# Kernel optimization log

Hardware: AMD Instinct MI355X
Metric: run time of the kernel (lower is better)

The kernel has to match this reference:

```python
import jax, jax.numpy as jnp
import numpy as np

EMBED_DIM = 1024
NUM_HEADS = 16
HEAD_DIM = EMBED_DIM // NUM_HEADS


def setup_inputs() -> dict:
    key = jax.random.key(0)
    k1, k2, k3, k4, k5 = jax.random.split(key, 5)
    x = jax.random.normal(k1, (4, 2048, EMBED_DIM), dtype=jnp.float32)
    # nn.Linear params: weight [out, in], bias [out]
    s_in = 1.0 / np.sqrt(EMBED_DIM)
    W_qkv = jax.random.uniform(k2, (3 * EMBED_DIM, EMBED_DIM), jnp.float32, -s_in, s_in)
    b_qkv = jax.random.uniform(k3, (3 * EMBED_DIM,), jnp.float32, -s_in, s_in)
    W_out = jax.random.uniform(k4, (EMBED_DIM, EMBED_DIM), jnp.float32, -s_in, s_in)
    b_out = jax.random.uniform(k5, (EMBED_DIM,), jnp.float32, -s_in, s_in)
    return {"x": x, "W_qkv": W_qkv, "b_qkv": b_qkv, "W_out": W_out, "b_out": b_out}


def reference(x, W_qkv, b_qkv, W_out, b_out):
    B, S, D = x.shape
    H, Dh = NUM_HEADS, HEAD_DIM
    qkv = x @ W_qkv.T + b_qkv                      # [B, S, 3D]
    qkv = qkv.reshape(B, S, 3, H, Dh)
    q = qkv[:, :, 0].transpose(0, 2, 1, 3)        # [B, H, S, Dh]
    k = qkv[:, :, 1].transpose(0, 2, 1, 3)
    v = qkv[:, :, 2].transpose(0, 2, 1, 3)
    scale = 1.0 / jnp.sqrt(jnp.asarray(Dh, x.dtype))
    scores = jnp.einsum('bhqd,bhkd->bhqk', q, k) * scale  # [B, H, S, S]
    attn = jax.nn.softmax(scores, axis=-1)
    out = jnp.einsum('bhqk,bhkd->bhqd', attn, v)  # [B, H, S, Dh]
    out = out.transpose(0, 2, 1, 3).reshape(B, S, D)
    return out @ W_out.T + b_out
```

## Files before the change

kernel.cpp:

```cpp
#include <hip/hip_runtime.h>

#define BB 4
#define SS 2048
#define DD 1024
#define HH 16
#define DHH 64
#define MM (BB*SS)

typedef __bf16 bf16x8 __attribute__((ext_vector_type(8)));
typedef float  f32x4  __attribute__((ext_vector_type(4)));

__device__ __forceinline__ unsigned short f2bf(float x) {
    unsigned int u = __float_as_uint(x);
    u += 0x7FFFu + ((u >> 16) & 1u);
    return (unsigned short)(u >> 16);
}

__global__ __launch_bounds__(256) void cvt_all(
    const float4* __restrict__ x,  const float4* __restrict__ wq,
    const float4* __restrict__ wo,
    ushort4* __restrict__ xb, ushort4* __restrict__ wqb, ushort4* __restrict__ wob)
{
    int i = blockIdx.x * 256 + threadIdx.x;
    const float4* src; ushort4* dst; int j;
    if (i < 2097152)      { src = x;  dst = xb;  j = i; }
    else if (i < 2883584) { src = wq; dst = wqb; j = i - 2097152; }
    else                  { src = wo; dst = wob; j = i - 2883584; }
    float4 v = src[j];
    ushort4 o;
    o.x = f2bf(v.x); o.y = f2bf(v.y); o.z = f2bf(v.z); o.w = f2bf(v.w);
    dst[j] = o;
}

__global__ __launch_bounds__(256) void qkv_gemm(
    const __bf16* __restrict__ A,
    const __bf16* __restrict__ W,
    const float* __restrict__ bias,
    __bf16* __restrict__ Qp,
    __bf16* __restrict__ Kp,
    __bf16* __restrict__ Vp)
{
    __shared__ __bf16 smem[2 * 128 * 72];
#define AS(r,c) smem[(r)*72 + (c)]
#define BS(r,c) smem[128*72 + (r)*72 + (c)]
#define CT(r,c) smem[(r)*132 + (c)]
    const int tid  = threadIdx.x;
    const int m0   = blockIdx.x * 128;
    const int n0   = blockIdx.y * 128;
    const int lane = tid & 63;
    const int wid  = tid >> 6;
    const int fr   = lane & 15;
    const int quad = lane >> 4;
    const int wm   = (wid >> 1) * 64;
    const int wn   = (wid & 1) * 64;

    f32x4 acc[4][4] = {};

    for (int k0 = 0; k0 < DD; k0 += 64) {
        __syncthreads();
        #pragma unroll
        for (int p = 0; p < 4; ++p) {
            int g = tid + p * 256;
            int r = g >> 3;
            int c = (g & 7) << 3;
            *(uint4*)&AS(r, c) = *(const uint4*)(A + (size_t)(m0 + r) * DD + k0 + c);
            *(uint4*)&BS(r, c) = *(const uint4*)(W + (size_t)(n0 + r) * DD + k0 + c);
        }
        __syncthreads();

        bf16x8 af[2][4], bw[2][4];
        #pragma unroll
        for (int kc = 0; kc < 2; ++kc)
            #pragma unroll
            for (int t = 0; t < 4; ++t) {
                af[kc][t] = *(const bf16x8*)&AS(wm + t*16 + fr, kc*32 + quad*8);
                bw[kc][t] = *(const bf16x8*)&BS(wn + t*16 + fr, kc*32 + quad*8);
            }
        #pragma unroll
        for (int kc = 0; kc < 2; ++kc)
            #pragma unroll
            for (int mt = 0; mt < 4; ++mt)
                #pragma unroll
                for (int nt = 0; nt < 4; ++nt)
                    acc[mt][nt] = __builtin_amdgcn_mfma_f32_16x16x32_bf16(
                        af[kc][mt], bw[kc][nt], acc[mt][nt], 0, 0, 0);
    }

    __syncthreads();
    const int t3 = n0 >> 10;
    const int b  = m0 >> 11;
    const int s0 = m0 & (SS - 1);

    float bn[4];
    #pragma unroll
    for (int nt = 0; nt < 4; ++nt) bn[nt] = bias[n0 + wn + nt*16 + fr];

    if (t3 == 2) {
        #pragma unroll
        for (int nt = 0; nt < 4; ++nt)
            #pragma unroll
            for (int mt = 0; mt < 4; ++mt)
                #pragma unroll
                for (int i = 0; i < 4; ++i)
                    CT(wn + nt*16 + fr, wm + mt*16 + quad*4 + i) =
                        (__bf16)(acc[mt][nt][i] + bn[nt]);
        __syncthreads();
        const int pn0 = n0 - 2048;
        #pragma unroll
        for (int p = 0; p < 8; ++p) {
            int g = tid + p * 256;
            int r = g >> 4;
            int c = (g & 15) << 3;
            int pn = pn0 + r, h = pn >> 6, dh = pn & 63;
            *(uint4*)&Vp[((size_t)((b*HH + h)*DHH + dh))*SS + s0 + c] = *(uint4*)&CT(r, c);
        }
    } else {
        __bf16* dst = (t3 == 0) ? Qp : Kp;
        const float qscale = (t3 == 0) ? 0.125f : 1.0f;
        #pragma unroll
        for (int nt = 0; nt < 4; ++nt)
            #pragma unroll
            for (int mt = 0; mt < 4; ++mt)
                #pragma unroll
                for (int i = 0; i < 4; ++i)
                    CT(wm + mt*16 + quad*4 + i, wn + nt*16 + fr) =
                        (__bf16)((acc[mt][nt][i] + bn[nt]) * qscale);
        __syncthreads();
        const int pn0 = (t3 == 0) ? n0 : n0 - 1024;
        #pragma unroll
        for (int p = 0; p < 8; ++p) {
            int g = tid + p * 256;
            int r = g >> 4;
            int c = (g & 15) << 3;
            int pn = pn0 + c, h = pn >> 6, dh = pn & 63;
            *(uint4*)&dst[((size_t)((b*HH + h))*SS + s0 + r)*DHH + dh] = *(uint4*)&CT(r, c);
        }
    }
#undef AS
#undef BS
#undef CT
}

__global__ __launch_bounds__(256) void out_gemm(
    const __bf16* __restrict__ A,
    const __bf16* __restrict__ W,
    const float* __restrict__ bias,
    float* __restrict__ out)
{
    __shared__ __bf16 As[128][72];
    __shared__ __bf16 Bs[128][72];
    const int tid  = threadIdx.x;
    const int m0   = blockIdx.x * 128;
    const int n0   = blockIdx.y * 128;
    const int lane = tid & 63;
    const int wid  = tid >> 6;
    const int fr   = lane & 15;
    const int quad = lane >> 4;
    const int wm   = (wid >> 1) * 64;
    const int wn   = (wid & 1) * 64;

    f32x4 acc[4][4] = {};

    for (int k0 = 0; k0 < DD; k0 += 64) {
        __syncthreads();
        #pragma unroll
        for (int p = 0; p < 4; ++p) {
            int g = tid + p * 256;
            int r = g >> 3;
            int c = (g & 7) << 3;
            *(uint4*)&As[r][c] = *(const uint4*)(A + (size_t)(m0 + r) * DD + k0 + c);
            *(uint4*)&Bs[r][c] = *(const uint4*)(W + (size_t)(n0 + r) * DD + k0 + c);
        }
        __syncthreads();

        bf16x8 af[2][4], bw[2][4];
        #pragma unroll
        for (int kc = 0; kc < 2; ++kc)
            #pragma unroll
            for (int t = 0; t < 4; ++t) {
                af[kc][t] = *(const bf16x8*)&As[wm + t*16 + fr][kc*32 + quad*8];
                bw[kc][t] = *(const bf16x8*)&Bs[wn + t*16 + fr][kc*32 + quad*8];
            }
        #pragma unroll
        for (int kc = 0; kc < 2; ++kc)
            #pragma unroll
            for (int mt = 0; mt < 4; ++mt)
                #pragma unroll
                for (int nt = 0; nt < 4; ++nt)
                    acc[mt][nt] = __builtin_amdgcn_mfma_f32_16x16x32_bf16(
                        af[kc][mt], bw[kc][nt], acc[mt][nt], 0, 0, 0);
    }

    #pragma unroll
    for (int nt = 0; nt < 4; ++nt) {
        int n  = n0 + wn + nt*16 + fr;
        float bnv = bias[n];
        #pragma unroll
        for (int mt = 0; mt < 4; ++mt) {
            #pragma unroll
            for (int i = 0; i < 4; ++i) {
                int m = m0 + wm + mt*16 + quad*4 + i;
                out[(size_t)m * DD + n] = acc[mt][nt][i] + bnv;
            }
        }
    }
}

__global__ __launch_bounds__(256, 2) void attn_mfma(
    const __bf16* __restrict__ Qp,
    const __bf16* __restrict__ Kp,
    const __bf16* __restrict__ Vp,
    __bf16* __restrict__ Op)
{
    __shared__ __bf16 Ks[128][72];
    __shared__ __bf16 VT[64][136];
    __shared__ __bf16 QPs[256][72];

    const int tid  = threadIdx.x;
    const int q0   = blockIdx.x * 256;
    const int bh   = blockIdx.y;
    const size_t base = (size_t)bh * SS * DHH;
    const int lane = tid & 63;
    const int wid  = tid >> 6;
    const int fr   = lane & 15;
    const int quad = lane >> 4;
    const int wrow = wid * 64;

    #pragma unroll
    for (int p = 0; p < 8; ++p) {
        int g = tid + p * 256;
        int r = g >> 3;
        int c = (g & 7) << 3;
        *(uint4*)&QPs[r][c] = *(const uint4*)(Qp + base + (size_t)(q0 + r) * DHH + c);
    }
    __syncthreads();

    bf16x8 aq[4][2];
    #pragma unroll
    for (int mt = 0; mt < 4; ++mt)
        #pragma unroll
        for (int kc = 0; kc < 2; ++kc)
            aq[mt][kc] = *(const bf16x8*)&QPs[wrow + mt*16 + fr][kc*32 + quad*8];

    f32x4 o[4][4] = {};
    float lp[4][4] = {};

    for (int kt = 0; kt < SS; kt += 128) {
        __syncthreads();
        #pragma unroll
        for (int p = 0; p < 4; ++p) {
            int g  = tid + p * 256;
            int rk = g >> 3;
            int ck = (g & 7) << 3;
            *(uint4*)&Ks[rk][ck] = *(const uint4*)(Kp + base + (size_t)(kt + rk) * DHH + ck);
            int dv = g >> 4;
            int cv = (g & 15) << 3;
            *(uint4*)&VT[dv][cv] = *(const uint4*)(Vp + base + (size_t)dv * SS + kt + cv);
        }
        __syncthreads();

        #pragma unroll
        for (int half = 0; half < 2; ++half) {
            const int koff = half * 64;

            #pragma unroll
            for (int mt = 0; mt < 4; ++mt) {
                f32x4 s[4] = {};
                #pragma unroll
                for (int nt = 0; nt < 4; ++nt)
                    #pragma unroll
                    for (int kc = 0; kc < 2; ++kc) {
                        bf16x8 bk = *(const bf16x8*)&Ks[koff + nt*16 + fr][kc*32 + quad*8];
                        s[nt] = __builtin_amdgcn_mfma_f32_16x16x32_bf16(
                            aq[mt][kc], bk, s[nt], 0, 0, 0);
                    }
                #pragma unroll
                for (int i = 0; i < 4; ++i) {
                    float e0 = __expf(s[0][i]);
                    float e1 = __expf(s[1][i]);
                    float e2 = __expf(s[2][i]);
                    float e3 = __expf(s[3][i]);
                    lp[mt][i] += (e0 + e1) + (e2 + e3);
                    QPs[wrow + mt*16 + quad*4 + i][0*16 + fr] = (__bf16)e0;
                    QPs[wrow + mt*16 + quad*4 + i][1*16 + fr] = (__bf16)e1;
                    QPs[wrow + mt*16 + quad*4 + i][2*16 + fr] = (__bf16)e2;
                    QPs[wrow + mt*16 + quad*4 + i][3*16 + fr] = (__bf16)e3;
                }
            }

            #pragma unroll
            for (int mt = 0; mt < 4; ++mt) {
                bf16x8 ap[2];
                #pragma unroll
                for (int kc = 0; kc < 2; ++kc)
                    ap[kc] = *(const bf16x8*)&QPs[wrow + mt*16 + fr][kc*32 + quad*8];
                #pragma unroll
                for (int nt = 0; nt < 4; ++nt)
                    #pragma unroll
                    for (int kc = 0; kc < 2; ++kc) {
                        bf16x8 bv = *(const bf16x8*)&VT[nt*16 + fr][koff + kc*32 + quad*8];
                        o[mt][nt] = __builtin_amdgcn_mfma_f32_16x16x32_bf16(
                            ap[kc], bv, o[mt][nt], 0, 0, 0);
                    }
            }
        }
    }

    __syncthreads();
    #pragma unroll
    for (int mt = 0; mt < 4; ++mt)
        #pragma unroll
        for (int i = 0; i < 4; ++i) {
            float v = lp[mt][i];
            v += __shfl_xor(v, 1);
            v += __shfl_xor(v, 2);
            v += __shfl_xor(v, 4);
            v += __shfl_xor(v, 8);
            float inv = 1.0f / v;
            #pragma unroll
            for (int nt = 0; nt < 4; ++nt)
                QPs[wrow + mt*16 + quad*4 + i][nt*16 + fr] = (__bf16)(o[mt][nt][i] * inv);
        }
    __syncthreads();

    const int b = bh >> 4, h = bh & (HH - 1);
    #pragma unroll
    for (int p = 0; p < 8; ++p) {
        int g = tid + p * 256;
        int r = g >> 3;
        int c = (g & 7) << 3;
        *(uint4*)&Op[((size_t)(b*SS + q0 + r))*DD + h*DHH + c] = *(uint4*)&QPs[r][c];
    }
}


extern "C" void kernel_launch(void* const* d_in, const int* in_sizes, int n_in,
                              void* d_out, int out_size, void* d_ws, size_t ws_size,
                              hipStream_t stream)
{
    const float* x     = (const float*)d_in[0];
    const float* W_qkv = (const float*)d_in[1];
    const float* b_qkv = (const float*)d_in[2];
    const float* W_out = (const float*)d_in[3];
    const float* b_out = (const float*)d_in[4];
    float* out = (float*)d_out;

    __bf16* ws  = (__bf16*)d_ws;
    __bf16* xb  = ws;
    __bf16* wqb = xb  + (size_t)8388608;
    __bf16* wob = wqb + (size_t)3145728;
    __bf16* qp  = wob + (size_t)1048576;
    __bf16* kp  = qp  + (size_t)8388608;
    __bf16* vp  = kp  + (size_t)8388608;
    __bf16* op  = vp  + (size_t)8388608;

    cvt_all<<<12288, 256, 0, stream>>>(
        (const float4*)x, (const float4*)W_qkv, (const float4*)W_out,
        (ushort4*)xb, (ushort4*)wqb, (ushort4*)wob);

    qkv_gemm<<<dim3(MM/128, 3*DD/128), 256, 0, stream>>>(xb, wqb, b_qkv, qp, kp, vp);
    attn_mfma<<<dim3(SS/256, BB*HH), 256, 0, stream>>>(qp, kp, vp, op);
    out_gemm<<<dim3(MM/128, DD/128), 256, 0, stream>>>(op, wob, b_out, out);
}
```

Baseline: 316.1 us.

## Use direct global-to-LDS loads with XOR-swizzled tiles and exp2 softmax

Replaces register-staged global-to-shared copies in both GEMMs and the attention kernel with global_load_lds 16-byte direct transfers. The shared tiles move from padded rows to an unpadded, rotation-swizzled layout, and fragment reads use the matching swizzle to avoid bank conflicts. K and V fragments are hoisted out of the mt loop in attention. The log2(e) factor is folded into the Q scale so the softmax can use the hardware exp2. This cuts VGPR traffic and LDS reads, but it depends on the per-lane LDS address pattern of global_load_lds matching the swizzle.

```diff
diff --git a/kernel.cpp b/kernel.cpp
--- a/kernel.cpp
+++ b/kernel.cpp
@@ -14,6 +14,12 @@
     unsigned int u = __float_as_uint(x);
     u += 0x7FFFu + ((u >> 16) & 1u);
     return (unsigned short)(u >> 16);
+}
+
+__device__ __forceinline__ void glds16(const __bf16* g, __bf16* l) {
+    __builtin_amdgcn_global_load_lds(
+        (const __attribute__((address_space(1))) void*)g,
+        (__attribute__((address_space(3))) void*)l, 16, 0, 0);
 }
 
 __global__ __launch_bounds__(256) void cvt_all(
@@ -40,10 +46,10 @@
     __bf16* __restrict__ Kp,
     __bf16* __restrict__ Vp)
 {
-    __shared__ __bf16 smem[2 * 128 * 72];
-#define AS(r,c) smem[(r)*72 + (c)]
-#define BS(r,c) smem[128*72 + (r)*72 + (c)]
+    __shared__ __bf16 smem[16896];
 #define CT(r,c) smem[(r)*132 + (c)]
+    __bf16* As = smem;
+    __bf16* Bs = smem + 8192;
     const int tid  = threadIdx.x;
     const int m0   = blockIdx.x * 128;
     const int n0   = blockIdx.y * 128;
@@ -54,17 +60,19 @@
     const int wm   = (wid >> 1) * 64;
     const int wn   = (wid & 1) * 64;
 
+    const int srow = lane >> 3;
+    const int sg   = ((lane & 7) - srow) & 7;
+
     f32x4 acc[4][4] = {};
 
     for (int k0 = 0; k0 < DD; k0 += 64) {
         __syncthreads();
         #pragma unroll
         for (int p = 0; p < 4; ++p) {
-            int g = tid + p * 256;
-            int r = g >> 3;
-            int c = (g & 7) << 3;
-            *(uint4*)&AS(r, c) = *(const uint4*)(A + (size_t)(m0 + r) * DD + k0 + c);
-            *(uint4*)&BS(r, c) = *(const uint4*)(W + (size_t)(n0 + r) * DD + k0 + c);
+            int cidx = p * 4 + wid;
+            int r = cidx * 8 + srow;
+            glds16(A + (size_t)(m0 + r) * DD + k0 + sg * 8, As + cidx * 512);
+            glds16(W + (size_t)(n0 + r) * DD + k0 + sg * 8, Bs + cidx * 512);
         }
         __syncthreads();
 
@@ -73,8 +81,9 @@
         for (int kc = 0; kc < 2; ++kc)
             #pragma unroll
             for (int t = 0; t < 4; ++t) {
-                af[kc][t] = *(const bf16x8*)&AS(wm + t*16 + fr, kc*32 + quad*8);
-                bw[kc][t] = *(const bf16x8*)&BS(wn + t*16 + fr, kc*32 + quad*8);
+                int col = ((kc * 4 + quad + fr) & 7) * 8;
+                af[kc][t] = *(const bf16x8*)&As[(wm + t*16 + fr) * 64 + col];
+                bw[kc][t] = *(const bf16x8*)&Bs[(wn + t*16 + fr) * 64 + col];
             }
         #pragma unroll
         for (int kc = 0; kc < 2; ++kc)
@@ -116,7 +125,7 @@
         }
     } else {
         __bf16* dst = (t3 == 0) ? Qp : Kp;
-        const float qscale = (t3 == 0) ? 0.125f : 1.0f;
+        const float qscale = (t3 == 0) ? 0.125f * 1.44269504088896340736f : 1.0f;
         #pragma unroll
         for (int nt = 0; nt < 4; ++nt)
             #pragma unroll
@@ -136,8 +145,6 @@
             *(uint4*)&dst[((size_t)((b*HH + h))*SS + s0 + r)*DHH + dh] = *(uint4*)&CT(r, c);
         }
     }
-#undef AS
-#undef BS
 #undef CT
 }
 
@@ -147,8 +154,9 @@
     const float* __restrict__ bias,
     float* __restrict__ out)
 {
-    __shared__ __bf16 As[128][72];
-    __shared__ __bf16 Bs[128][72];
+    __shared__ __bf16 smem[16384];
+    __bf16* As = smem;
+    __bf16* Bs = smem + 8192;
     const int tid  = threadIdx.x;
     const int m0   = blockIdx.x * 128;
     const int n0   = blockIdx.y * 128;
@@ -159,17 +167,19 @@
     const int wm   = (wid >> 1) * 64;
     const int wn   = (wid & 1) * 64;
 
+    const int srow = lane >> 3;
+    const int sg   = ((lane & 7) - srow) & 7;
+
     f32x4 acc[4][4] = {};
 
     for (int k0 = 0; k0 < DD; k0 += 64) {
         __syncthreads();
         #pragma unroll
         for (int p = 0; p < 4; ++p) {
-            int g = tid + p * 256;
-            int r = g >> 3;
-            int c = (g & 7) << 3;
-            *(uint4*)&As[r][c] = *(const uint4*)(A + (size_t)(m0 + r) * DD + k0 + c);
-            *(uint4*)&Bs[r][c] = *(const uint4*)(W + (size_t)(n0 + r) * DD + k0 + c);
+            int cidx = p * 4 + wid;
+            int r = cidx * 8 + srow;
+            glds16(A + (size_t)(m0 + r) * DD + k0 + sg * 8, As + cidx * 512);
+            glds16(W + (size_t)(n0 + r) * DD + k0 + sg * 8, Bs + cidx * 512);
         }
         __syncthreads();
 
@@ -178,8 +188,9 @@
         for (int kc = 0; kc < 2; ++kc)
             #pragma unroll
             for (int t = 0; t < 4; ++t) {
-                af[kc][t] = *(const bf16x8*)&As[wm + t*16 + fr][kc*32 + quad*8];
-                bw[kc][t] = *(const bf16x8*)&Bs[wn + t*16 + fr][kc*32 + quad*8];
+                int col = ((kc * 4 + quad + fr) & 7) * 8;
+                af[kc][t] = *(const bf16x8*)&As[(wm + t*16 + fr) * 64 + col];
+                bw[kc][t] = *(const bf16x8*)&Bs[(wn + t*16 + fr) * 64 + col];
             }
         #pragma unroll
         for (int kc = 0; kc < 2; ++kc)
@@ -212,8 +223,8 @@
     const __bf16* __restrict__ Vp,
     __bf16* __restrict__ Op)
 {
-    __shared__ __bf16 Ks[128][72];
-    __shared__ __bf16 VT[64][136];
+    __shared__ __bf16 Ks[128 * 64];
+    __shared__ __bf16 VT[64 * 128];
     __shared__ __bf16 QPs[256][72];
 
     const int tid  = threadIdx.x;
@@ -226,6 +237,11 @@
     const int quad = lane >> 4;
     const int wrow = wid * 64;
 
+    const int srowK = lane >> 3;
+    const int sgK   = ((lane & 7) - srowK) & 7;
+    const int srowV = lane >> 4;
+    const int sgV0  = lane & 15;
+
     #pragma unroll
     for (int p = 0; p < 8; ++p) {
         int g = tid + p * 256;
@@ -249,13 +265,12 @@
         __syncthreads();
         #pragma unroll
         for (int p = 0; p < 4; ++p) {
-            int g  = tid + p * 256;
-            int rk = g >> 3;
-            int ck = (g & 7) << 3;
-            *(uint4*)&Ks[rk][ck] = *(const uint4*)(Kp + base + (size_t)(kt + rk) * DHH + ck);
-            int dv = g >> 4;
-            int cv = (g & 15) << 3;
-            *(uint4*)&VT[dv][cv] = *(const uint4*)(Vp + base + (size_t)dv * SS + kt + cv);
+            int cidx = p * 4 + wid;
+            int rk = cidx * 8 + srowK;
+            glds16(Kp + base + (size_t)(kt + rk) * DHH + sgK * 8, Ks + cidx * 512);
+            int rv = cidx * 4 + srowV;
+            int gv = (sgV0 - rv) & 15;
+            glds16(Vp + base + (size_t)rv * SS + kt + gv * 8, VT + cidx * 512);
         }
         __syncthreads();
 
@@ -263,23 +278,29 @@
         for (int half = 0; half < 2; ++half) {
             const int koff = half * 64;
 
+            bf16x8 bk[4][2];
+            #pragma unroll
+            for (int nt = 0; nt < 4; ++nt)
+                #pragma unroll
+                for (int kc = 0; kc < 2; ++kc)
+                    bk[nt][kc] = *(const bf16x8*)
+                        &Ks[(koff + nt*16 + fr) * 64 + ((kc*4 + quad + fr) & 7) * 8];
+
             #pragma unroll
             for (int mt = 0; mt < 4; ++mt) {
                 f32x4 s[4] = {};
                 #pragma unroll
                 for (int nt = 0; nt < 4; ++nt)
                     #pragma unroll
-                    for (int kc = 0; kc < 2; ++kc) {
-                        bf16x8 bk = *(const bf16x8*)&Ks[koff + nt*16 + fr][kc*32 + quad*8];
+                    for (int kc = 0; kc < 2; ++kc)
                         s[nt] = __builtin_amdgcn_mfma_f32_16x16x32_bf16(
-                            aq[mt][kc], bk, s[nt], 0, 0, 0);
-                    }
+                            aq[mt][kc], bk[nt][kc], s[nt], 0, 0, 0);
                 #pragma unroll
                 for (int i = 0; i < 4; ++i) {
-                    float e0 = __expf(s[0][i]);
-                    float e1 = __expf(s[1][i]);
-                    float e2 = __expf(s[2][i]);
-                    float e3 = __expf(s[3][i]);
+                    float e0 = __builtin_amdgcn_exp2f(s[0][i]);
+                    float e1 = __builtin_amdgcn_exp2f(s[1][i]);
+                    float e2 = __builtin_amdgcn_exp2f(s[2][i]);
+                    float e3 = __builtin_amdgcn_exp2f(s[3][i]);
                     lp[mt][i] += (e0 + e1) + (e2 + e3);
                     QPs[wrow + mt*16 + quad*4 + i][0*16 + fr] = (__bf16)e0;
                     QPs[wrow + mt*16 + quad*4 + i][1*16 + fr] = (__bf16)e1;
@@ -288,6 +309,14 @@
                 }
             }
 
+            bf16x8 bv[4][2];
+            #pragma unroll
+            for (int nt = 0; nt < 4; ++nt)
+                #pragma unroll
+                for (int kc = 0; kc < 2; ++kc)
+                    bv[nt][kc] = *(const bf16x8*)
+                        &VT[(nt*16 + fr) * 128 + ((half*8 + kc*4 + quad + fr) & 15) * 8];
+
             #pragma unroll
             for (int mt = 0; mt < 4; ++mt) {
                 bf16x8 ap[2];
@@ -297,11 +326,9 @@
                 #pragma unroll
                 for (int nt = 0; nt < 4; ++nt)
                     #pragma unroll
-                    for (int kc = 0; kc < 2; ++kc) {
-                        bf16x8 bv = *(const bf16x8*)&VT[nt*16 + fr][koff + kc*32 + quad*8];
+                    for (int kc = 0; kc < 2; ++kc)
                         o[mt][nt] = __builtin_amdgcn_mfma_f32_16x16x32_bf16(
-                            ap[kc], bv, o[mt][nt], 0, 0, 0);
-                    }
+                            ap[kc], bv[nt][kc], o[mt][nt], 0, 0, 0);
             }
         }
     }
```

Result: slower. 354.2 us (+12.1%).
